# Performance work log

Measured on AMD Instinct MI355X. Metric: run time of the kernel, lower is better.

The kernel has to match this reference:

```python
import jax, jax.numpy as jnp
import numpy as np

INPUT_SIZE, OUTPUT_SIZE, HIDDEN, NUM_LAYERS, T = 32, 10, 1536, 2, 64


def _lstm_cell(x, h, c, W_ih, W_hh, b_ih, b_hh):
    # PyTorch LSTMCell: gates ordered i, f, g, o
    g = x @ W_ih.T + b_ih + h @ W_hh.T + b_hh
    i_, f_, g_, o_ = jnp.split(g, 4, axis=-1)
    c2 = jax.nn.sigmoid(f_) * c + jax.nn.sigmoid(i_) * jnp.tanh(g_)
    h2 = jax.nn.sigmoid(o_) * jnp.tanh(c2)
    return h2, c2


def setup_inputs() -> dict:
    key = jax.random.key(0)
    ks = jax.random.split(key, 16)
    s = 1.0 / np.sqrt(HIDDEN)
    u = lambda k, shape: jax.random.uniform(k, shape, jnp.float32, -s, s)
    return {
        "inputs": jax.random.normal(ks[0], (T, 1, INPUT_SIZE), jnp.float32),
        "h_init": jnp.zeros((NUM_LAYERS, 1, HIDDEN), jnp.float32),
        "c_init": jnp.zeros((NUM_LAYERS, 1, HIDDEN), jnp.float32),
        "W_ih0": u(ks[1], (4 * HIDDEN, INPUT_SIZE)),
        "W_hh0": u(ks[2], (4 * HIDDEN, HIDDEN)),
        "b_ih0": u(ks[3], (4 * HIDDEN,)),
        "b_hh0": u(ks[4], (4 * HIDDEN,)),
        "W_ih1": u(ks[5], (4 * HIDDEN, HIDDEN)),
        "W_hh1": u(ks[6], (4 * HIDDEN, HIDDEN)),
        "b_ih1": u(ks[7], (4 * HIDDEN,)),
        "b_hh1": u(ks[8], (4 * HIDDEN,)),
        "W_lin": u(ks[9], (OUTPUT_SIZE, HIDDEN)),
        "b_lin": u(ks[10], (OUTPUT_SIZE,)),
        "lookup": jnp.asarray(np.linspace(0.1, 1.0, OUTPUT_SIZE), jnp.float32),
    }


def reference(inputs, h_init, c_init, W_ih0, W_hh0, b_ih0, b_hh0,
              W_ih1, W_hh1, b_ih1, b_hh1, W_lin, b_lin, lookup):
    S = T * INPUT_SIZE  # total sequential sub-steps
    keys = jax.random.split(jax.random.key(42), S)
    iidx = jnp.arange(S) // INPUT_SIZE  # timestep index
    jidx = jnp.arange(S) % INPUT_SIZE   # feature sub-step index
    pos = jnp.arange(INPUT_SIZE)

    def step(carry, xs):
        h0, c0, h1, c1, x_aug = carry
        k, i, j = xs
        # fresh input at the start of each timestep (j == 0)
        x = jnp.where(j == 0, inputs[i], x_aug)  # [1, INPUT_SIZE]
        h0, c0 = _lstm_cell(x, h0, c0, W_ih0, W_hh0, b_ih0, b_hh0)
        h1, c1 = _lstm_cell(h0, h1, c1, W_ih1, W_hh1, b_ih1, b_hh1)
        logits = h1 @ W_lin.T + b_lin          # [1, OUTPUT_SIZE]
        probs = jax.nn.softmax(logits, -1)
        action = jax.random.categorical(k, logits, axis=-1)  # [1] int
        scale = jnp.where(j == 0, 1.0, lookup[action])        # [1]
        # mult: ones except position j scaled by lookup[action]
        new_x = x * jnp.where(pos[None, :] == j, scale[:, None], 1.0)
        return (h0, c0, h1, c1, new_x), (action, probs)

    carry0 = (h_init[0], c_init[0], h_init[1], c_init[1], inputs[0])
    _, (actions, probs) = jax.lax.scan(step, carry0, (keys, iidx, jidx))
    return actions, probs  # [S,1] int, [S,1,OUTPUT_SIZE] float
```

## Files before the change

### kernel.cpp

```cpp
#include <hip/hip_runtime.h>
#include <math.h>

#define NWG   256
#define TPB   512
#define H     1536
#define S_TOT 2048
#define RPW   6
#define GRW   24
#define OUTP  2048

#define SMEM_FLOATS (10 * H + 8 * H)
#define SMEM_BYTES  (SMEM_FLOATS * 4)

struct F4 { float x, y, z, w; };

struct Params {
  const float* inputs; const float* h_init; const float* c_init;
  const float* W_ih0; const float* W_hh0; const float* b_ih0; const float* b_hh0;
  const float* W_ih1; const float* W_hh1; const float* b_ih1; const float* b_hh1;
  const float* W_lin; const float* b_lin; const float* lookup;
  float* out; float* h0g; float* h1g; unsigned* bar;
};

__device__ __forceinline__ float gload(const float* p) {
  return __hip_atomic_load(p, __ATOMIC_RELAXED, __HIP_MEMORY_SCOPE_AGENT);
}
__device__ __forceinline__ void gstore(float* p, float v) {
  __hip_atomic_store(p, v, __ATOMIC_RELAXED, __HIP_MEMORY_SCOPE_AGENT);
}

__device__ __forceinline__ void tf2x32(unsigned k0, unsigned k1,
                                       unsigned x0, unsigned x1,
                                       unsigned& o0, unsigned& o1) {
  unsigned ks2 = k0 ^ k1 ^ 0x1BD11BDAu;
  x0 += k0; x1 += k1;
#define TFR(r) { x0 += x1; x1 = ((x1 << r) | (x1 >> (32 - r))); x1 ^= x0; }
  TFR(13) TFR(15) TFR(26) TFR(6)   x0 += k1;  x1 += ks2 + 1u;
  TFR(17) TFR(29) TFR(16) TFR(24)  x0 += ks2; x1 += k0 + 2u;
  TFR(13) TFR(15) TFR(26) TFR(6)   x0 += k0;  x1 += k1 + 3u;
  TFR(17) TFR(29) TFR(16) TFR(24)  x0 += k1;  x1 += ks2 + 4u;
  TFR(13) TFR(15) TFR(26) TFR(6)   x0 += ks2; x1 += k0 + 5u;
#undef TFR
  o0 = x0; o1 = x1;
}

__device__ __forceinline__ double bsum64(double v) {
#pragma unroll
  for (int o = 32; o > 0; o >>= 1) v += __shfl_xor(v, o);
  return v;
}

__device__ __forceinline__ float sigf(float x) { return 1.0f / (1.0f + expf(-x)); }

__device__ __forceinline__ void flagbar(unsigned* bar, unsigned e, int tid, int wg) {
  __builtin_amdgcn_fence(__ATOMIC_RELEASE, "agent");
  __syncthreads();
  if (tid == 0)
    __hip_atomic_store(&bar[wg], e, __ATOMIC_RELEASE, __HIP_MEMORY_SCOPE_AGENT);
  if (tid < 64) {
    const unsigned* f = bar + tid * 4;
    bool done;
    do {
      int d0 = (int)(__hip_atomic_load(f + 0, __ATOMIC_RELAXED, __HIP_MEMORY_SCOPE_AGENT) - e);
      int d1 = (int)(__hip_atomic_load(f + 1, __ATOMIC_RELAXED, __HIP_MEMORY_SCOPE_AGENT) - e);
      int d2 = (int)(__hip_atomic_load(f + 2, __ATOMIC_RELAXED, __HIP_MEMORY_SCOPE_AGENT) - e);
      int d3 = (int)(__hip_atomic_load(f + 3, __ATOMIC_RELAXED, __HIP_MEMORY_SCOPE_AGENT) - e);
      done = ((d0 | d1 | d2 | d3) >= 0);
    } while (!__all(done));
    __builtin_amdgcn_fence(__ATOMIC_ACQUIRE, "agent");
  }
  __syncthreads();
}

__global__
__attribute__((amdgpu_flat_work_group_size(TPB, TPB), amdgpu_waves_per_eu(2, 2)))
void lstm_persistent(Params P) {
  const int tid  = threadIdx.x;
  const int wg   = blockIdx.x;
  const int wv   = tid >> 6;
  const int lane = tid & 63;

  extern __shared__ float smem[];
  float* s_Wlin = smem;
  float* s_W3   = smem + 10 * H;

  __shared__ float s_Wih0[GRW * 32];
  __shared__ float s_h0[H], s_h1[H];
  __shared__ float s_bih0[GRW], s_bhh0[GRW], s_bih1[GRW], s_bhh1[GRW];
  __shared__ float s_hh1dot[GRW], s_gate[GRW];
  __shared__ float s_x[32];
  __shared__ float s_c0[RPW], s_c1[RPW];
  __shared__ float s_logits[16];
  __shared__ float s_blin[10], s_lookup[10];
  __shared__ int   s_action;

  for (int k = tid; k < GRW * 32; k += TPB) {
    int idx = k >> 5, kk = k & 31;
    int q = idx / RPW, u = idx % RPW;
    int gr = q * H + wg * RPW + u;
    s_Wih0[k] = P.W_ih0[gr * 32 + kk];
  }
  for (int k = tid; k < 10 * H; k += TPB) s_Wlin[k] = P.W_lin[k];
  for (int k = tid; k < 8 * H; k += TPB) {
    int w8 = k / H, col = k % H;
    int idx = w8 * 3 + 2;
    int q = idx / RPW, u = idx % RPW;
    int gr = q * H + wg * RPW + u;
    s_W3[k] = P.W_ih1[(size_t)gr * H + col];
  }
  if (tid < GRW) {
    int q = tid / RPW, u = tid % RPW;
    int gr = q * H + wg * RPW + u;
    s_bih0[tid] = P.b_ih0[gr]; s_bhh0[tid] = P.b_hh0[gr];
    s_bih1[tid] = P.b_ih1[gr]; s_bhh1[tid] = P.b_hh1[gr];
  }
  if (tid < 10) { s_blin[tid] = P.b_lin[tid]; s_lookup[tid] = P.lookup[tid]; }
  if (tid < RPW) {
    s_c0[tid] = P.c_init[wg * RPW + tid];
    s_c1[tid] = P.c_init[H + wg * RPW + tid];
    gstore(P.h0g + wg * RPW + tid, P.h_init[wg * RPW + tid]);
    gstore(P.h1g + wg * RPW + tid, P.h_init[H + wg * RPW + tid]);
  }

#define ROWP(M, IDX) ((M) + (size_t)((((IDX) / RPW) * H) + wg * RPW + ((IDX) % RPW)) * H)
  const float* p00 = ROWP(P.W_hh0, wv * 3 + 0);
  const float* p01 = ROWP(P.W_hh0, wv * 3 + 1);
  const float* p02 = ROWP(P.W_hh0, wv * 3 + 2);
  const float* p10 = ROWP(P.W_hh1, wv * 3 + 0);
  const float* p11 = ROWP(P.W_hh1, wv * 3 + 1);
  const float* p12 = ROWP(P.W_hh1, wv * 3 + 2);
  const float* p20 = ROWP(P.W_ih1, wv * 3 + 0);
  const float* p21 = ROWP(P.W_ih1, wv * 3 + 1);
#undef ROWP
#define MK4(p, g) F4{ (p)[lane + ((4*(g)+0) << 6)], (p)[lane + ((4*(g)+1) << 6)], \
                      (p)[lane + ((4*(g)+2) << 6)], (p)[lane + ((4*(g)+3) << 6)] }
#define DECLROW(v, p) F4 v##0 = MK4(p,0), v##1 = MK4(p,1), v##2 = MK4(p,2), \
                         v##3 = MK4(p,3), v##4 = MK4(p,4), v##5 = MK4(p,5)
  DECLROW(w0_, p00); DECLROW(w1_, p01); DECLROW(w2_, p02);
  DECLROW(w3_, p10); DECLROW(w4_, p11); DECLROW(w5_, p12);
  DECLROW(w6_, p20); DECLROW(w7_, p21);
#undef DECLROW
#undef MK4

  unsigned ep = 1;
  flagbar(P.bar, ep++, tid, wg);

  for (int s = 0; s <= S_TOT; ++s) {
#pragma unroll
    for (int r = 0; r < 3; ++r) {
      int k = tid + r * TPB;
      s_h0[k] = gload(P.h0g + k);
      s_h1[k] = gload(P.h1g + k);
    }
    __syncthreads();

    if (s > 0) {
      int sp = s - 1;
#pragma unroll
      for (int p2 = 0; p2 < 2; ++p2) {
        int l = wv + 8 * p2;
        if (l < 10) {
          double acc = 0.0;
#pragma unroll
          for (int t = 0; t < 24; ++t) {
            int off = lane + (t << 6);
            acc += (double)s_Wlin[l * H + off] * (double)s_h1[off];
          }
          acc = bsum64(acc);
          if (lane == 0) s_logits[l] = __fadd_rn((float)acc, s_blin[l]);
        }
      }
      __syncthreads();

      if (wv == 0) {
        unsigned kk0, kk1; tf2x32(0u, 42u, 0u, (unsigned)sp, kk0, kk1);
        unsigned b1, b2; tf2x32(kk0, kk1, 0u, (unsigned)lane, b1, b2);
        unsigned bits = b1 ^ b2;
        float uraw = __fsub_rn(__uint_as_float((bits >> 9) | 0x3F800000u), 1.0f);
        const float TINY = 1.17549435e-38f;
        float u  = fmaxf(TINY, __fadd_rn(uraw, TINY));
        float gum = -logf(-logf(u));
        float lg = (lane < 10) ? s_logits[lane] : 0.0f;
        float y  = (lane < 10) ? __fadd_rn(lg, gum) : -INFINITY;
        int ai = lane;
#pragma unroll
        for (int o = 1; o < 16; o <<= 1) {
          float oy = __shfl_xor(y, o); int oi = __shfl_xor(ai, o);
          if (oy > y || (oy == y && oi < ai)) { y = oy; ai = oi; }
        }
        float lm = (lane < 10) ? lg : -INFINITY;
#pragma unroll
        for (int o = 1; o < 16; o <<= 1) lm = fmaxf(lm, __shfl_xor(lm, o));
        float e2 = (lane < 10) ? expf(__fsub_rn(lg, lm)) : 0.0f;
        float ssum = e2;
#pragma unroll
        for (int o = 1; o < 16; o <<= 1) ssum = __fadd_rn(ssum, __shfl_xor(ssum, o));
        if (lane == 0) s_action = ai;
        if (wg == 0) {
          if (lane < 10) P.out[OUTP + sp * 10 + lane] = e2 / ssum;
          if (lane == 0) P.out[sp] = (float)ai;
        }
      }
      __syncthreads();
      if (tid == 0) {
        int jp = sp & 31;
        if (jp != 0) s_x[jp] = __fmul_rn(s_x[jp], s_lookup[s_action]);
      }
      __syncthreads();
    }

    if (s == S_TOT) break;
    int ii = s >> 5, jj = s & 31;
    if (jj == 0 && tid < 32) s_x[tid] = P.inputs[ii * 32 + tid];
    __syncthreads();

    {
      double a0 = 0, a1 = 0, a2 = 0, b0 = 0, b1 = 0, b2 = 0;
#define GRP1(g) { \
      const int off = lane + ((g) << 8); \
      const double h00 = (double)s_h0[off],       h01 = (double)s_h0[off + 64], \
                   h02 = (double)s_h0[off + 128], h03 = (double)s_h0[off + 192]; \
      const double h10 = (double)s_h1[off],       h11 = (double)s_h1[off + 64], \
                   h12 = (double)s_h1[off + 128], h13 = (double)s_h1[off + 192]; \
      a0 += (double)w0_##g.x * h00; a0 += (double)w0_##g.y * h01; a0 += (double)w0_##g.z * h02; a0 += (double)w0_##g.w * h03; \
      a1 += (double)w1_##g.x * h00; a1 += (double)w1_##g.y * h01; a1 += (double)w1_##g.z * h02; a1 += (double)w1_##g.w * h03; \
      a2 += (double)w2_##g.x * h00; a2 += (double)w2_##g.y * h01; a2 += (double)w2_##g.z * h02; a2 += (double)w2_##g.w * h03; \
      b0 += (double)w3_##g.x * h10; b0 += (double)w3_##g.y * h11; b0 += (double)w3_##g.z * h12; b0 += (double)w3_##g.w * h13; \
      b1 += (double)w4_##g.x * h10; b1 += (double)w4_##g.y * h11; b1 += (double)w4_##g.z * h12; b1 += (double)w4_##g.w * h13; \
      b2 += (double)w5_##g.x * h10; b2 += (double)w5_##g.y * h11; b2 += (double)w5_##g.z * h12; b2 += (double)w5_##g.w * h13; \
      }
      GRP1(0) GRP1(1) GRP1(2) GRP1(3) GRP1(4) GRP1(5)
#undef GRP1
      a0 = bsum64(a0); a1 = bsum64(a1); a2 = bsum64(a2);
      b0 = bsum64(b0); b1 = bsum64(b1); b2 = bsum64(b2);
      double xa0, xa1, xa2;
#define XDOT(slot, dst) { \
      double pp = (lane < 32) \
        ? (double)s_Wih0[(((wv * 3 + (slot)) << 5) + lane)] * (double)s_x[lane] : 0.0; \
      pp += __shfl_xor(pp, 16); pp += __shfl_xor(pp, 8); pp += __shfl_xor(pp, 4); \
      pp += __shfl_xor(pp, 2);  pp += __shfl_xor(pp, 1); \
      dst = pp; }
      XDOT(0, xa0) XDOT(1, xa1) XDOT(2, xa2)
#undef XDOT
      if (lane == 0) {
#define WB1(slot, xav, aav, bbv) { \
        const int idx = wv * 3 + (slot); \
        float g0 = __fadd_rn(__fadd_rn(__fadd_rn((float)(xav), s_bih0[idx]), \
                                       (float)(aav)), s_bhh0[idx]); \
        s_gate[idx] = g0; s_hh1dot[idx] = (float)(bbv); }
        WB1(0, xa0, a0, b0) WB1(1, xa1, a1, b1) WB1(2, xa2, a2, b2)
#undef WB1
      }
    }
    __syncthreads();
    if (tid < RPW) {
      int u = tid;
      float gi = s_gate[u], gf = s_gate[6 + u], gg = s_gate[12 + u], go = s_gate[18 + u];
      float c = __fadd_rn(__fmul_rn(sigf(gf), s_c0[u]), __fmul_rn(sigf(gi), tanhf(gg)));
      s_c0[u] = c;
      float h = __fmul_rn(sigf(go), tanhf(c));
      gstore(P.h0g + wg * RPW + u, h);
    }
    flagbar(P.bar, ep++, tid, wg);

#pragma unroll
    for (int r = 0; r < 3; ++r) {
      int k = tid + r * TPB;
      s_h0[k] = gload(P.h0g + k);
    }
    __syncthreads();
    {
      double a0 = 0, a1 = 0, a2 = 0;
      const int w3b = wv * H;
#define GRP2(g) { \
      const int off = lane + ((g) << 8); \
      const double h00 = (double)s_h0[off],       h01 = (double)s_h0[off + 64], \
                   h02 = (double)s_h0[off + 128], h03 = (double)s_h0[off + 192]; \
      a0 += (double)w6_##g.x * h00; a0 += (double)w6_##g.y * h01; a0 += (double)w6_##g.z * h02; a0 += (double)w6_##g.w * h03; \
      a1 += (double)w7_##g.x * h00; a1 += (double)w7_##g.y * h01; a1 += (double)w7_##g.z * h02; a1 += (double)w7_##g.w * h03; \
      a2 += (double)s_W3[w3b + off] * h00;       a2 += (double)s_W3[w3b + off + 64] * h01; \
      a2 += (double)s_W3[w3b + off + 128] * h02; a2 += (double)s_W3[w3b + off + 192] * h03; \
      }
      GRP2(0) GRP2(1) GRP2(2) GRP2(3) GRP2(4) GRP2(5)
#undef GRP2
      a0 = bsum64(a0); a1 = bsum64(a1); a2 = bsum64(a2);
      if (lane == 0) {
#define WB2(slot, aav) { \
        const int idx = wv * 3 + (slot); \
        s_gate[idx] = __fadd_rn(__fadd_rn(__fadd_rn((float)(aav), s_bih1[idx]), \
                                          s_hh1dot[idx]), s_bhh1[idx]); }
        WB2(0, a0) WB2(1, a1) WB2(2, a2)
#undef WB2
      }
    }
    __syncthreads();
    if (tid < RPW) {
      int u = tid;
      float gi = s_gate[u], gf = s_gate[6 + u], gg = s_gate[12 + u], go = s_gate[18 + u];
      float c = __fadd_rn(__fmul_rn(sigf(gf), s_c1[u]), __fmul_rn(sigf(gi), tanhf(gg)));
      s_c1[u] = c;
      float h = __fmul_rn(sigf(go), tanhf(c));
      gstore(P.h1g + wg * RPW + u, h);
    }
    flagbar(P.bar, ep++, tid, wg);
  }
}

extern "C" void kernel_launch(void* const* d_in, const int* in_sizes, int n_in,
                              void* d_out, int out_size, void* d_ws, size_t ws_size,
                              hipStream_t stream) {
  (void)in_sizes; (void)n_in; (void)out_size; (void)ws_size;
  Params p;
  p.inputs = (const float*)d_in[0];
  p.h_init = (const float*)d_in[1];
  p.c_init = (const float*)d_in[2];
  p.W_ih0  = (const float*)d_in[3];
  p.W_hh0  = (const float*)d_in[4];
  p.b_ih0  = (const float*)d_in[5];
  p.b_hh0  = (const float*)d_in[6];
  p.W_ih1  = (const float*)d_in[7];
  p.W_hh1  = (const float*)d_in[8];
  p.b_ih1  = (const float*)d_in[9];
  p.b_hh1  = (const float*)d_in[10];
  p.W_lin  = (const float*)d_in[11];
  p.b_lin  = (const float*)d_in[12];
  p.lookup = (const float*)d_in[13];
  p.out    = (float*)d_out;
  float* ws = (float*)d_ws;
  p.h0g = ws;
  p.h1g = ws + H;
  p.bar = (unsigned*)(ws + 2 * H);

  hipFuncSetAttribute((const void*)lstm_persistent,
                      hipFuncAttributeMaxDynamicSharedMemorySize, SMEM_BYTES);
  hipLaunchKernelGGL(lstm_persistent, dim3(NWG), dim3(TPB), SMEM_BYTES, stream, p);
}
```

Before: 186.3 ms.

## Double workgroup to 1024 threads, split hh0/hh1 across waves, move W_ih1 to LDS

Workgroups grow from 512 to 1024 threads. Waves 0-7 now compute the W_hh0 dots and waves 8-15 the W_hh1 dots, so each wave keeps only 3 rows in registers instead of 8, and the layer-0 phase gets more parallelism. The layer-1 W_ih1 rows move almost entirely into LDS (23 rows), with the last row read from global memory. W_lin is now streamed from global memory each step instead of held in LDS. The aim is to shorten the per-step critical path, at the cost of more LDS and global traffic in the layer-1 phase, which waves 8-15 now leave idle.

```diff
diff --git a/kernel.cpp b/kernel.cpp
--- a/kernel.cpp
+++ b/kernel.cpp
@@ -1,16 +1,16 @@
 #include <hip/hip_runtime.h>
 #include <math.h>
 
-#define NWG   256
-#define TPB   512
-#define H     1536
-#define S_TOT 2048
-#define RPW   6
-#define GRW   24
-#define OUTP  2048
-
-#define SMEM_FLOATS (10 * H + 8 * H)
-#define SMEM_BYTES  (SMEM_FLOATS * 4)
+#define NWG    256
+#define TPB    1024
+#define H      1536
+#define S_TOT  2048
+#define RPW    6
+#define GRW    24
+#define OUTP   2048
+#define W3ROWS 23
+
+#define SMEM_BYTES (W3ROWS * H * 4)
 
 struct F4 { float x, y, z, w; };
 
@@ -73,7 +73,7 @@
 }
 
 __global__
-__attribute__((amdgpu_flat_work_group_size(TPB, TPB), amdgpu_waves_per_eu(2, 2)))
+__attribute__((amdgpu_flat_work_group_size(TPB, TPB), amdgpu_waves_per_eu(4, 4)))
 void lstm_persistent(Params P) {
   const int tid  = threadIdx.x;
   const int wg   = blockIdx.x;
@@ -81,8 +81,7 @@
   const int lane = tid & 63;
 
   extern __shared__ float smem[];
-  float* s_Wlin = smem;
-  float* s_W3   = smem + 10 * H;
+  float* s_W3 = smem;
 
   __shared__ float s_Wih0[GRW * 32];
   __shared__ float s_h0[H], s_h1[H];
@@ -100,12 +99,9 @@
     int gr = q * H + wg * RPW + u;
     s_Wih0[k] = P.W_ih0[gr * 32 + kk];
   }
-  for (int k = tid; k < 10 * H; k += TPB) s_Wlin[k] = P.W_lin[k];
-  for (int k = tid; k < 8 * H; k += TPB) {
-    int w8 = k / H, col = k % H;
-    int idx = w8 * 3 + 2;
-    int q = idx / RPW, u = idx % RPW;
-    int gr = q * H + wg * RPW + u;
+  for (int k = tid; k < W3ROWS * H; k += TPB) {
+    int r = k / H, col = k % H;
+    int gr = (r / RPW) * H + wg * RPW + (r % RPW);
     s_W3[k] = P.W_ih1[(size_t)gr * H + col];
   }
   if (tid < GRW) {
@@ -123,32 +119,29 @@
   }
 
 #define ROWP(M, IDX) ((M) + (size_t)((((IDX) / RPW) * H) + wg * RPW + ((IDX) % RPW)) * H)
-  const float* p00 = ROWP(P.W_hh0, wv * 3 + 0);
-  const float* p01 = ROWP(P.W_hh0, wv * 3 + 1);
-  const float* p02 = ROWP(P.W_hh0, wv * 3 + 2);
-  const float* p10 = ROWP(P.W_hh1, wv * 3 + 0);
-  const float* p11 = ROWP(P.W_hh1, wv * 3 + 1);
-  const float* p12 = ROWP(P.W_hh1, wv * 3 + 2);
-  const float* p20 = ROWP(P.W_ih1, wv * 3 + 0);
-  const float* p21 = ROWP(P.W_ih1, wv * 3 + 1);
+  const int abase = (wv < 8) ? (wv * 3) : ((wv - 8) * 3);
+  const float* Wbig = (wv < 8) ? P.W_hh0 : P.W_hh1;
+  const float* q0 = ROWP(Wbig, abase + 0);
+  const float* q1 = ROWP(Wbig, abase + 1);
+  const float* q2 = ROWP(Wbig, abase + 2);
+  const float* pW23 = ROWP(P.W_ih1, 23);
+  const float* pLin = P.W_lin + (size_t)((wv < 10) ? wv : 0) * H;
 #undef ROWP
 #define MK4(p, g) F4{ (p)[lane + ((4*(g)+0) << 6)], (p)[lane + ((4*(g)+1) << 6)], \
                       (p)[lane + ((4*(g)+2) << 6)], (p)[lane + ((4*(g)+3) << 6)] }
-#define DECLROW(v, p) F4 v##0 = MK4(p,0), v##1 = MK4(p,1), v##2 = MK4(p,2), \
-                         v##3 = MK4(p,3), v##4 = MK4(p,4), v##5 = MK4(p,5)
-  DECLROW(w0_, p00); DECLROW(w1_, p01); DECLROW(w2_, p02);
-  DECLROW(w3_, p10); DECLROW(w4_, p11); DECLROW(w5_, p12);
-  DECLROW(w6_, p20); DECLROW(w7_, p21);
-#undef DECLROW
+  F4 r0_0 = MK4(q0,0), r0_1 = MK4(q0,1), r0_2 = MK4(q0,2),
+     r0_3 = MK4(q0,3), r0_4 = MK4(q0,4), r0_5 = MK4(q0,5);
+  F4 r1_0 = MK4(q1,0), r1_1 = MK4(q1,1), r1_2 = MK4(q1,2),
+     r1_3 = MK4(q1,3), r1_4 = MK4(q1,4), r1_5 = MK4(q1,5);
+  F4 r2_0 = MK4(q2,0), r2_1 = MK4(q2,1), r2_2 = MK4(q2,2),
+     r2_3 = MK4(q2,3), r2_4 = MK4(q2,4), r2_5 = MK4(q2,5);
 #undef MK4
 
   unsigned ep = 1;
   flagbar(P.bar, ep++, tid, wg);
 
   for (int s = 0; s <= S_TOT; ++s) {
-#pragma unroll
-    for (int r = 0; r < 3; ++r) {
-      int k = tid + r * TPB;
+    for (int k = tid; k < H; k += TPB) {
       s_h0[k] = gload(P.h0g + k);
       s_h1[k] = gload(P.h1g + k);
     }
@@ -156,19 +149,15 @@
 
     if (s > 0) {
       int sp = s - 1;
-#pragma unroll
-      for (int p2 = 0; p2 < 2; ++p2) {
-        int l = wv + 8 * p2;
-        if (l < 10) {
-          double acc = 0.0;
-#pragma unroll
-          for (int t = 0; t < 24; ++t) {
-            int off = lane + (t << 6);
-            acc += (double)s_Wlin[l * H + off] * (double)s_h1[off];
-          }
-          acc = bsum64(acc);
-          if (lane == 0) s_logits[l] = __fadd_rn((float)acc, s_blin[l]);
-        }
+      if (wv < 10) {
+        double acc = 0.0;
+#pragma unroll
+        for (int t = 0; t < 24; ++t) {
+          const int off = lane + (t << 6);
+          acc += (double)gload(pLin + off) * (double)s_h1[off];
+        }
+        acc = bsum64(acc);
+        if (lane == 0) s_logits[wv] = __fadd_rn((float)acc, s_blin[wv]);
       }
       __syncthreads();
 
@@ -215,41 +204,44 @@
     __syncthreads();
 
     {
-      double a0 = 0, a1 = 0, a2 = 0, b0 = 0, b1 = 0, b2 = 0;
-#define GRP1(g) { \
+      const float* hsrc = (wv < 8) ? s_h0 : s_h1;
+      double a0 = 0, a1 = 0, a2 = 0;
+#define GRPH(g) { \
       const int off = lane + ((g) << 8); \
-      const double h00 = (double)s_h0[off],       h01 = (double)s_h0[off + 64], \
-                   h02 = (double)s_h0[off + 128], h03 = (double)s_h0[off + 192]; \
-      const double h10 = (double)s_h1[off],       h11 = (double)s_h1[off + 64], \
-                   h12 = (double)s_h1[off + 128], h13 = (double)s_h1[off + 192]; \
-      a0 += (double)w0_##g.x * h00; a0 += (double)w0_##g.y * h01; a0 += (double)w0_##g.z * h02; a0 += (double)w0_##g.w * h03; \
-      a1 += (double)w1_##g.x * h00; a1 += (double)w1_##g.y * h01; a1 += (double)w1_##g.z * h02; a1 += (double)w1_##g.w * h03; \
-      a2 += (double)w2_##g.x * h00; a2 += (double)w2_##g.y * h01; a2 += (double)w2_##g.z * h02; a2 += (double)w2_##g.w * h03; \
-      b0 += (double)w3_##g.x * h10; b0 += (double)w3_##g.y * h11; b0 += (double)w3_##g.z * h12; b0 += (double)w3_##g.w * h13; \
-      b1 += (double)w4_##g.x * h10; b1 += (double)w4_##g.y * h11; b1 += (double)w4_##g.z * h12; b1 += (double)w4_##g.w * h13; \
-      b2 += (double)w5_##g.x * h10; b2 += (double)w5_##g.y * h11; b2 += (double)w5_##g.z * h12; b2 += (double)w5_##g.w * h13; \
-      }
-      GRP1(0) GRP1(1) GRP1(2) GRP1(3) GRP1(4) GRP1(5)
-#undef GRP1
+      const double hv0 = (double)hsrc[off],       hv1 = (double)hsrc[off + 64], \
+                   hv2 = (double)hsrc[off + 128], hv3 = (double)hsrc[off + 192]; \
+      a0 += (double)r0_##g.x * hv0; a0 += (double)r0_##g.y * hv1; a0 += (double)r0_##g.z * hv2; a0 += (double)r0_##g.w * hv3; \
+      a1 += (double)r1_##g.x * hv0; a1 += (double)r1_##g.y * hv1; a1 += (double)r1_##g.z * hv2; a1 += (double)r1_##g.w * hv3; \
+      a2 += (double)r2_##g.x * hv0; a2 += (double)r2_##g.y * hv1; a2 += (double)r2_##g.z * hv2; a2 += (double)r2_##g.w * hv3; \
+      }
+      GRPH(0) GRPH(1) GRPH(2) GRPH(3) GRPH(4) GRPH(5)
+#undef GRPH
       a0 = bsum64(a0); a1 = bsum64(a1); a2 = bsum64(a2);
-      b0 = bsum64(b0); b1 = bsum64(b1); b2 = bsum64(b2);
-      double xa0, xa1, xa2;
+      if (wv < 8) {
+        double xa0, xa1, xa2;
 #define XDOT(slot, dst) { \
-      double pp = (lane < 32) \
-        ? (double)s_Wih0[(((wv * 3 + (slot)) << 5) + lane)] * (double)s_x[lane] : 0.0; \
-      pp += __shfl_xor(pp, 16); pp += __shfl_xor(pp, 8); pp += __shfl_xor(pp, 4); \
-      pp += __shfl_xor(pp, 2);  pp += __shfl_xor(pp, 1); \
-      dst = pp; }
-      XDOT(0, xa0) XDOT(1, xa1) XDOT(2, xa2)
+        double pp = (lane < 32) \
+          ? (double)s_Wih0[(((wv * 3 + (slot)) << 5) + lane)] * (double)s_x[lane] : 0.0; \
+        pp += __shfl_xor(pp, 16); pp += __shfl_xor(pp, 8); pp += __shfl_xor(pp, 4); \
+        pp += __shfl_xor(pp, 2);  pp += __shfl_xor(pp, 1); \
+        dst = pp; }
+        XDOT(0, xa0) XDOT(1, xa1) XDOT(2, xa2)
 #undef XDOT
-      if (lane == 0) {
-#define WB1(slot, xav, aav, bbv) { \
-        const int idx = wv * 3 + (slot); \
-        float g0 = __fadd_rn(__fadd_rn(__fadd_rn((float)(xav), s_bih0[idx]), \
-                                       (float)(aav)), s_bhh0[idx]); \
-        s_gate[idx] = g0; s_hh1dot[idx] = (float)(bbv); }
-        WB1(0, xa0, a0, b0) WB1(1, xa1, a1, b1) WB1(2, xa2, a2, b2)
+        if (lane == 0) {
+#define WB1(slot, xav, aav) { \
+          const int idx = wv * 3 + (slot); \
+          s_gate[idx] = __fadd_rn(__fadd_rn(__fadd_rn((float)(xav), s_bih0[idx]), \
+                                            (float)(aav)), s_bhh0[idx]); }
+          WB1(0, xa0, a0) WB1(1, xa1, a1) WB1(2, xa2, a2)
 #undef WB1
+        }
+      } else {
+        if (lane == 0) {
+          const int idx = (wv - 8) * 3;
+          s_hh1dot[idx]     = (float)a0;
+          s_hh1dot[idx + 1] = (float)a1;
+          s_hh1dot[idx + 2] = (float)a2;
+        }
       }
     }
     __syncthreads();
@@ -263,26 +255,24 @@
     }
     flagbar(P.bar, ep++, tid, wg);
 
-#pragma unroll
-    for (int r = 0; r < 3; ++r) {
-      int k = tid + r * TPB;
-      s_h0[k] = gload(P.h0g + k);
-    }
-    __syncthreads();
-    {
+    for (int k = tid; k < H; k += TPB) s_h0[k] = gload(P.h0g + k);
+    __syncthreads();
+    if (wv < 7) {
+      const int rb0 = (wv * 3) * H, rb1 = rb0 + H, rb2 = rb1 + H;
       double a0 = 0, a1 = 0, a2 = 0;
-      const int w3b = wv * H;
-#define GRP2(g) { \
+#define GRPL(g) { \
       const int off = lane + ((g) << 8); \
-      const double h00 = (double)s_h0[off],       h01 = (double)s_h0[off + 64], \
-                   h02 = (double)s_h0[off + 128], h03 = (double)s_h0[off + 192]; \
-      a0 += (double)w6_##g.x * h00; a0 += (double)w6_##g.y * h01; a0 += (double)w6_##g.z * h02; a0 += (double)w6_##g.w * h03; \
-      a1 += (double)w7_##g.x * h00; a1 += (double)w7_##g.y * h01; a1 += (double)w7_##g.z * h02; a1 += (double)w7_##g.w * h03; \
-      a2 += (double)s_W3[w3b + off] * h00;       a2 += (double)s_W3[w3b + off + 64] * h01; \
-      a2 += (double)s_W3[w3b + off + 128] * h02; a2 += (double)s_W3[w3b + off + 192] * h03; \
-      }
-      GRP2(0) GRP2(1) GRP2(2) GRP2(3) GRP2(4) GRP2(5)
-#undef GRP2
+      const double hv0 = (double)s_h0[off],       hv1 = (double)s_h0[off + 64], \
+                   hv2 = (double)s_h0[off + 128], hv3 = (double)s_h0[off + 192]; \
+      a0 += (double)s_W3[rb0 + off] * hv0;       a0 += (double)s_W3[rb0 + off + 64] * hv1; \
+      a0 += (double)s_W3[rb0 + off + 128] * hv2; a0 += (double)s_W3[rb0 + off + 192] * hv3; \
+      a1 += (double)s_W3[rb1 + off] * hv0;       a1 += (double)s_W3[rb1 + off + 64] * hv1; \
+      a1 += (double)s_W3[rb1 + off + 128] * hv2; a1 += (double)s_W3[rb1 + off + 192] * hv3; \
+      a2 += (double)s_W3[rb2 + off] * hv0;       a2 += (double)s_W3[rb2 + off + 64] * hv1; \
+      a2 += (double)s_W3[rb2 + off + 128] * hv2; a2 += (double)s_W3[rb2 + off + 192] * hv3; \
+      }
+      GRPL(0) GRPL(1) GRPL(2) GRPL(3) GRPL(4) GRPL(5)
+#undef GRPL
       a0 = bsum64(a0); a1 = bsum64(a1); a2 = bsum64(a2);
       if (lane == 0) {
 #define WB2(slot, aav) { \
@@ -291,6 +281,30 @@
                                           s_hh1dot[idx]), s_bhh1[idx]); }
         WB2(0, a0) WB2(1, a1) WB2(2, a2)
 #undef WB2
+      }
+    } else if (wv == 7) {
+      const int rb0 = 21 * H, rb1 = 22 * H;
+      double a0 = 0, a1 = 0, a2 = 0;
+#define GRPE(g) { \
+      const int off = lane + ((g) << 8); \
+      const double hv0 = (double)s_h0[off],       hv1 = (double)s_h0[off + 64], \
+                   hv2 = (double)s_h0[off + 128], hv3 = (double)s_h0[off + 192]; \
+      a0 += (double)s_W3[rb0 + off] * hv0;       a0 += (double)s_W3[rb0 + off + 64] * hv1; \
+      a0 += (double)s_W3[rb0 + off + 128] * hv2; a0 += (double)s_W3[rb0 + off + 192] * hv3; \
+      a1 += (double)s_W3[rb1 + off] * hv0;       a1 += (double)s_W3[rb1 + off + 64] * hv1; \
+      a1 += (double)s_W3[rb1 + off + 128] * hv2; a1 += (double)s_W3[rb1 + off + 192] * hv3; \
+      a2 += (double)gload(pW23 + off) * hv0;       a2 += (double)gload(pW23 + off + 64) * hv1; \
+      a2 += (double)gload(pW23 + off + 128) * hv2; a2 += (double)gload(pW23 + off + 192) * hv3; \
+      }
+      GRPE(0) GRPE(1) GRPE(2) GRPE(3) GRPE(4) GRPE(5)
+#undef GRPE
+      a0 = bsum64(a0); a1 = bsum64(a1); a2 = bsum64(a2);
+      if (lane == 0) {
+#define WB2E(idx, aav) { \
+        s_gate[idx] = __fadd_rn(__fadd_rn(__fadd_rn((float)(aav), s_bih1[idx]), \
+                                          s_hh1dot[idx]), s_bhh1[idx]); }
+        WB2E(21, a0) WB2E(22, a1) WB2E(23, a2)
+#undef WB2E
       }
     }
     __syncthreads();
```

Measured after the change: 254.5 ms. +36.6%, slower.
